# Performance work log

Hardware: AMD Instinct MI355X
Metric: run time of the kernel (lower is better)

The kernel has to match this reference:

```python
import jax, jax.numpy as jnp
import numpy as np

DMODEL = 1024
N_MAMBAS = 4
D_INNER = 2 * DMODEL          # expand = 2
D_STATE = 16                  # mamba_ssm default
D_CONV = 4                    # mamba_ssm default
DT_RANK = DMODEL // 16        # ceil(d_model/16) = 64


def setup_inputs() -> dict:
    key = jax.random.key(0)
    ks = jax.random.split(key, 8)
    B, L, n = 2, 4096, N_MAMBAS
    f32 = jnp.float32
    x = jax.random.normal(ks[0], (B, L, DMODEL), f32)
    in_w = jax.random.normal(ks[1], (n, 2 * D_INNER, DMODEL), f32) * 0.02
    conv_w = jax.random.normal(ks[2], (n, D_INNER, D_CONV), f32) * 0.1
    conv_b = jnp.zeros((n, D_INNER), f32)
    xproj_w = jax.random.normal(ks[3], (n, DT_RANK + 2 * D_STATE, D_INNER), f32) * 0.02
    dt_w = jax.random.normal(ks[4], (n, D_INNER, DT_RANK), f32) * 0.02
    # softplus-inverse of dt_init ~ 0.01 (mamba-style dt bias init)
    dt_b = jnp.log(jnp.expm1(jnp.full((n, D_INNER), 0.01, f32)))
    # S4D-real init: A_log = log(1..d_state)
    A_log = jnp.log(jnp.broadcast_to(jnp.arange(1, D_STATE + 1, dtype=f32), (n, D_INNER, D_STATE)))
    D_skip = jnp.ones((n, D_INNER), f32)
    out_w = jax.random.normal(ks[5], (n, DMODEL, D_INNER), f32) * 0.02
    return dict(x=x, in_w=in_w, conv_w=conv_w, conv_b=conv_b, xproj_w=xproj_w,
                dt_w=dt_w, dt_b=dt_b, A_log=A_log, D_skip=D_skip, out_w=out_w)


def _mamba(x, in_w, conv_w, conv_b, xproj_w, dt_w, dt_b, A_log, D_skip, out_w):
    # x: (B, Lc, D)
    Bb = x.shape[0]
    xz = jnp.einsum('bld,ed->ble', x, in_w)                 # (B, Lc, 2*D_INNER)
    xi, z = jnp.split(xz, 2, axis=-1)
    # causal depthwise conv over time
    xc = jnp.transpose(xi, (0, 2, 1))                       # (B, D_INNER, Lc)
    xc = jax.lax.conv_general_dilated(xc, conv_w[:, None, :], (1,),
                                      [(D_CONV - 1, 0)], feature_group_count=D_INNER)
    xi = jax.nn.silu(jnp.transpose(xc + conv_b[None, :, None], (0, 2, 1)))  # (B, Lc, D_INNER)
    proj = jnp.einsum('bld,ed->ble', xi, xproj_w)           # (B, Lc, DT_RANK + 2*D_STATE)
    dt = proj[..., :DT_RANK]
    Bm = proj[..., DT_RANK:DT_RANK + D_STATE]
    Cm = proj[..., DT_RANK + D_STATE:]
    dt = jax.nn.softplus(jnp.einsum('blr,dr->bld', dt, dt_w) + dt_b)  # (B, Lc, D_INNER)
    A = -jnp.exp(A_log)                                     # (D_INNER, D_STATE)

    def step(h, inp):
        dt_t, B_t, C_t, x_t = inp                           # (B,Di),(B,Ds),(B,Ds),(B,Di)
        dA = jnp.exp(dt_t[:, :, None] * A)                  # (B, Di, Ds)
        h = dA * h + dt_t[:, :, None] * B_t[:, None, :] * x_t[:, :, None]
        return h, jnp.einsum('bds,bs->bd', h, C_t)

    h0 = jnp.zeros((Bb, D_INNER, D_STATE), x.dtype)
    xs_t = (jnp.swapaxes(dt, 0, 1), jnp.swapaxes(Bm, 0, 1),
            jnp.swapaxes(Cm, 0, 1), jnp.swapaxes(xi, 0, 1))
    _, ys = jax.lax.scan(step, h0, xs_t)                    # (Lc, B, D_INNER)
    y = jnp.swapaxes(ys, 0, 1) + xi * D_skip                # (B, Lc, D_INNER)
    y = y * jax.nn.silu(z)
    return jnp.einsum('ble,de->bld', y, out_w)              # (B, Lc, D)


def reference(x, in_w, conv_w, conv_b, xproj_w, dt_w, dt_b, A_log, D_skip, out_w):
    B, L, D = x.shape
    n = N_MAMBAS
    # strided slices x[:, i::n] == reshape(B, L//n, n, D)[:, :, i]
    xs = jnp.transpose(x.reshape(B, L // n, n, D), (2, 0, 1, 3))   # (n, B, Lc, D)
    ys = jax.vmap(_mamba)(xs, in_w, conv_w, conv_b, xproj_w,
                          dt_w, dt_b, A_log, D_skip, out_w)        # (n, B, Lc, D)
    # torch.cat(dim=1) concatenates per-mamba outputs block-wise along seq
    return jnp.transpose(ys, (1, 0, 2, 3)).reshape(B, L, D)
```

## Files before the change

### kernel.cpp

```cpp
#include <hip/hip_runtime.h>
#include <math.h>

#define DM   1024
#define DI   2048
#define DSn  16
#define DTR  64
#define PW   96
#define LS   1024
#define NCH  16
#define CL   64
#define XKS  8

typedef unsigned short u16;
typedef unsigned int   u32;
typedef __attribute__((ext_vector_type(8))) short bf16x8;
typedef __attribute__((ext_vector_type(8))) unsigned short u16x8;
typedef __attribute__((ext_vector_type(4))) float f32x4;

__device__ __forceinline__ void split2(float f, u16& hi, u16& lo) {
  union { float f; unsigned int u; } v; v.f = f;
  hi = (u16)(v.u >> 16);
  union { unsigned int u; float f; } w; w.u = v.u & 0xffff0000u;
  union { float f; unsigned int u; } r; r.f = f - w.f;
  lo = (u16)(r.u >> 16);
}

template<int ROWS>
__device__ __forceinline__ bf16x8 frag(const u16* T, int l4, int row) {
  return *(const bf16x8*)&T[(l4 * ROWS + row) * 8];
}

template<int ROWS>
__device__ __forceinline__ void stage16f(const float* a, u16* Th, u16* Tl, int ra, int half) {
  #pragma unroll
  for (int q = 0; q < 2; ++q) {
    u16x8 vh, vl;
    #pragma unroll
    for (int c = 0; c < 8; ++c) {
      u16 h_, l_;
      split2(a[q * 8 + c], h_, l_);
      vh[c] = h_; vl[c] = l_;
    }
    const int slot = ((half * 2 + q) * ROWS + ra) * 8;
    *(u16x8*)&Th[slot] = vh;
    *(u16x8*)&Tl[slot] = vl;
  }
}

template<int ROWS>
__device__ __forceinline__ void stage8f(const float* a, u16* Th, u16* Tl, int rb, int kq) {
  u16x8 vh, vl;
  #pragma unroll
  for (int c = 0; c < 8; ++c) {
    u16 h_, l_;
    split2(a[c], h_, l_);
    vh[c] = h_; vl[c] = l_;
  }
  const int slot = (kq * ROWS + rb) * 8;
  *(u16x8*)&Th[slot] = vh;
  *(u16x8*)&Tl[slot] = vl;
}

__global__ __launch_bounds__(256) void k_split_x(
    const float* __restrict__ x, u16* __restrict__ xh, u16* __restrict__ xl, int ib0)
{
  const int idx = blockIdx.x * 256 + threadIdx.x;
  const int t = idx >> 8, kq = (idx & 255) * 4;
  const int gt = ib0 * 1024 + t;
  const int j = gt & (LS - 1), ib = gt >> 10;
  const int i = ib >> 1, bb = ib & 1;
  const float4 v = *(const float4*)&x[(size_t)(bb * 4096 + j * 4 + i) * DM + kq];
  ushort4 vh, vl;
  split2(v.x, vh.x, vl.x); split2(v.y, vh.y, vl.y);
  split2(v.z, vh.z, vl.z); split2(v.w, vh.w, vl.w);
  *(ushort4*)&xh[(size_t)t * DM + kq] = vh;
  *(ushort4*)&xl[(size_t)t * DM + kq] = vl;
}

__global__ __launch_bounds__(512) void k_inproj(
    const u16* __restrict__ xh, const u16* __restrict__ xl,
    const float* __restrict__ inwf,
    float* __restrict__ xz, int ib0, int swz)
{
  __shared__ __align__(16) u16 Ah[4*256*8], Al[4*256*8];
  __shared__ __align__(16) u16 Bh[4*128*8], Bl[4*128*8];
  const int tid = threadIdx.x;
  int mblk, nblk;
  if (swz) {
    const int o = blockIdx.x;
    const int xcd = o & 7, within = o >> 3;
    const int il_ = xcd >> 1, nh = xcd & 1;
    mblk = il_ * 8 + (within & 7);
    nblk = nh * 16 + (within >> 3);
  } else {
    mblk = blockIdx.x; nblk = blockIdx.y;
  }
  const int m0 = mblk << 8, n0 = nblk << 7;
  const int ib = ib0 + (m0 >> 10);
  const int il = (ib >> 1) - (ib0 >> 1);
  const int ra = tid >> 1, half = tid & 1;
  const u16* Aph = xh + (size_t)(m0 + ra) * DM + half * 16;
  const u16* Apl = xl + (size_t)(m0 + ra) * DM + half * 16;
  const int rb = tid >> 2, kq = tid & 3;
  const float* Bpf = inwf + ((size_t)il * 4096 + n0 + rb) * DM + kq * 8;
  const int w = tid >> 6, lane = tid & 63;
  const int wr = w >> 1, wc = w & 1;
  const int l15 = lane & 15, l4 = lane >> 4;

  f32x4 acc[4][4];
  #pragma unroll
  for (int a_ = 0; a_ < 4; ++a_)
    #pragma unroll
    for (int b_ = 0; b_ < 4; ++b_) acc[a_][b_] = (f32x4)(0.f);

  u16x8 pa[4];
  float br[8];
  pa[0] = *(const u16x8*)(Aph);     pa[1] = *(const u16x8*)(Aph + 8);
  pa[2] = *(const u16x8*)(Apl);     pa[3] = *(const u16x8*)(Apl + 8);
  *(f32x4*)&br[0] = *(const f32x4*)(Bpf);
  *(f32x4*)&br[4] = *(const f32x4*)(Bpf + 4);
  const int nk = DM / 32;
  for (int kt = 0; kt < nk; ++kt) {
    __syncthreads();
    *(u16x8*)&Ah[((half*2+0)*256 + ra)*8] = pa[0];
    *(u16x8*)&Ah[((half*2+1)*256 + ra)*8] = pa[1];
    *(u16x8*)&Al[((half*2+0)*256 + ra)*8] = pa[2];
    *(u16x8*)&Al[((half*2+1)*256 + ra)*8] = pa[3];
    stage8f<128>(br, Bh, Bl, rb, kq);
    __syncthreads();
    if (kt + 1 < nk) {
      const int k0 = (kt + 1) * 32;
      pa[0] = *(const u16x8*)(Aph + k0);     pa[1] = *(const u16x8*)(Aph + k0 + 8);
      pa[2] = *(const u16x8*)(Apl + k0);     pa[3] = *(const u16x8*)(Apl + k0 + 8);
      *(f32x4*)&br[0] = *(const f32x4*)(Bpf + k0);
      *(f32x4*)&br[4] = *(const f32x4*)(Bpf + k0 + 4);
    }
    bf16x8 ah[4], al[4];
    #pragma unroll
    for (int mf = 0; mf < 4; ++mf) {
      const int row = wr * 64 + mf * 16 + l15;
      ah[mf] = frag<256>(Ah, l4, row);
      al[mf] = frag<256>(Al, l4, row);
    }
    #pragma unroll
    for (int nf = 0; nf < 4; ++nf) {
      const int col = wc * 64 + nf * 16 + l15;
      bf16x8 bh = frag<128>(Bh, l4, col);
      bf16x8 bl = frag<128>(Bl, l4, col);
      #pragma unroll
      for (int mf = 0; mf < 4; ++mf) {
        acc[mf][nf] = __builtin_amdgcn_mfma_f32_16x16x32_bf16(ah[mf], bh, acc[mf][nf], 0, 0, 0);
        acc[mf][nf] = __builtin_amdgcn_mfma_f32_16x16x32_bf16(ah[mf], bl, acc[mf][nf], 0, 0, 0);
        acc[mf][nf] = __builtin_amdgcn_mfma_f32_16x16x32_bf16(al[mf], bh, acc[mf][nf], 0, 0, 0);
      }
    }
  }
  #pragma unroll
  for (int mf = 0; mf < 4; ++mf) {
    const int row = m0 + wr * 64 + mf * 16 + l4 * 4;
    #pragma unroll
    for (int nf = 0; nf < 4; ++nf) {
      const int col = n0 + wc * 64 + nf * 16 + l15;
      #pragma unroll
      for (int r = 0; r < 4; ++r)
        xz[(size_t)(row + r) * (2 * DI) + col] = acc[mf][nf][r];
    }
  }
}

__global__ __launch_bounds__(256) void k_conv(
    const float* __restrict__ xz, const float* __restrict__ convw,
    const float* __restrict__ convb, float* __restrict__ xib,
    int ib0, int ntok)
{
  const int idx = blockIdx.x * 256 + threadIdx.x;
  if (idx >= ntok * (DI / 4)) return;
  const int t = idx / (DI / 4);
  const int c = (idx - t * (DI / 4)) * 4;
  const int j = t & (LS - 1);
  const int i = (ib0 + (t >> 10)) >> 1;
  float4 acc = *(const float4*)&convb[(size_t)i * DI + c];
  float4 wt[4];
  #pragma unroll
  for (int q = 0; q < 4; ++q)
    wt[q] = *(const float4*)&convw[((size_t)i * DI + c + q) * 4];
  #pragma unroll
  for (int k = 0; k < 4; ++k) {
    const int j2 = j + k - 3;
    if (j2 >= 0) {
      const float4 v = *(const float4*)&xz[(size_t)(t + k - 3) * (2 * DI) + c];
      acc.x = fmaf(v.x, ((const float*)&wt[0])[k], acc.x);
      acc.y = fmaf(v.y, ((const float*)&wt[1])[k], acc.y);
      acc.z = fmaf(v.z, ((const float*)&wt[2])[k], acc.z);
      acc.w = fmaf(v.w, ((const float*)&wt[3])[k], acc.w);
    }
  }
  float4 o;
  o.x = acc.x / (1.f + __expf(-acc.x));
  o.y = acc.y / (1.f + __expf(-acc.y));
  o.z = acc.z / (1.f + __expf(-acc.z));
  o.w = acc.w / (1.f + __expf(-acc.w));
  *(float4*)&xib[(size_t)t * DI + c] = o;
}

__global__ __launch_bounds__(256) void k_xproj_part(
    const float* __restrict__ xif, const float* __restrict__ xwf,
    float* __restrict__ Pp, int ib0, int ntok)
{
  __shared__ __align__(16) u16 Ah[4*64*8], Al[4*64*8];
  __shared__ __align__(16) u16 Bh[4*96*8], Bl[4*96*8];
  const int tid = threadIdx.x;
  const int m0 = blockIdx.x << 6;
  const int ks = blockIdx.y;
  const int kbase = ks * (DI / XKS);
  const int ib = ib0 + (m0 >> 10);
  const int il = (ib >> 1) - (ib0 >> 1);
  const int ra = tid >> 1, half = tid & 1;
  const bool hasA = (tid < 128);
  const bool hasB = (tid < 192);
  const float* Apf = xif + (size_t)(m0 + ra) * DI + kbase + half * 16;
  const float* Bpf = xwf + ((size_t)il * PW + ra) * DI + kbase + half * 16;
  const int w = tid >> 6, lane = tid & 63;
  const int l15 = lane & 15, l4 = lane >> 4;

  f32x4 acc[6];
  #pragma unroll
  for (int b_ = 0; b_ < 6; ++b_) acc[b_] = (f32x4)(0.f);

  float ar[16], br[16];
  if (hasA) {
    #pragma unroll
    for (int q = 0; q < 4; ++q) *(f32x4*)&ar[q*4] = *(const f32x4*)(Apf + q*4);
  }
  if (hasB) {
    #pragma unroll
    for (int q = 0; q < 4; ++q) *(f32x4*)&br[q*4] = *(const f32x4*)(Bpf + q*4);
  }
  const int nk = (DI / XKS) / 32;
  for (int kt = 0; kt < nk; ++kt) {
    __syncthreads();
    if (hasA) stage16f<64>(ar, Ah, Al, ra, half);
    if (hasB) stage16f<96>(br, Bh, Bl, ra, half);
    __syncthreads();
    if (kt + 1 < nk) {
      const int k0 = (kt + 1) * 32;
      if (hasA) {
        #pragma unroll
        for (int q = 0; q < 4; ++q) *(f32x4*)&ar[q*4] = *(const f32x4*)(Apf + k0 + q*4);
      }
      if (hasB) {
        #pragma unroll
        for (int q = 0; q < 4; ++q) *(f32x4*)&br[q*4] = *(const f32x4*)(Bpf + k0 + q*4);
      }
    }
    const int arow = w * 16 + l15;
    bf16x8 ah = frag<64>(Ah, l4, arow);
    bf16x8 al = frag<64>(Al, l4, arow);
    #pragma unroll
    for (int nf = 0; nf < 6; ++nf) {
      const int col = nf * 16 + l15;
      bf16x8 bh = frag<96>(Bh, l4, col);
      bf16x8 bl = frag<96>(Bl, l4, col);
      acc[nf] = __builtin_amdgcn_mfma_f32_16x16x32_bf16(ah, bh, acc[nf], 0, 0, 0);
      acc[nf] = __builtin_amdgcn_mfma_f32_16x16x32_bf16(ah, bl, acc[nf], 0, 0, 0);
      acc[nf] = __builtin_amdgcn_mfma_f32_16x16x32_bf16(al, bh, acc[nf], 0, 0, 0);
    }
  }
  float* outp = Pp + (size_t)ks * ntok * PW;
  const int row = m0 + w * 16 + l4 * 4;
  #pragma unroll
  for (int nf = 0; nf < 6; ++nf) {
    const int col = nf * 16 + l15;
    #pragma unroll
    for (int r = 0; r < 4; ++r)
      outp[(size_t)(row + r) * PW + col] = acc[nf][r];
  }
}

__global__ __launch_bounds__(256) void k_xproj_red(
    const float* __restrict__ Pp, float* __restrict__ projb, int ntok)
{
  const int idx = blockIdx.x * 256 + threadIdx.x;
  if (idx >= ntok * PW) return;
  const size_t plane = (size_t)ntok * PW;
  float s = 0.f;
  #pragma unroll
  for (int ks = 0; ks < XKS; ++ks) s += Pp[(size_t)ks * plane + idx];
  projb[idx] = s;
}

__global__ __launch_bounds__(256) void k_dtproj(
    const float* __restrict__ proj, const float* __restrict__ dtw,
    const float* __restrict__ dtbias, float* __restrict__ dtout,
    int dstride, int ib0)
{
  __shared__ float As[16][132];
  __shared__ float Bs[16][132];
  const int tid = threadIdx.x;
  const int n0 = blockIdx.x << 7;
  const int m0 = blockIdx.y << 7;
  const int ib = ib0 + (m0 >> 10);
  const int i  = ib >> 1;
  const int ar = tid >> 2, kq = tid & 3;
  const float* A0 = proj + (size_t)(m0 + ar) * PW + kq * 4;
  const float* A1 = A0 + (size_t)64 * PW;
  const float* Wb = dtw + (size_t)i * DI * DTR;
  const float* B0 = Wb + (size_t)(n0 + ar) * DTR + kq * 4;
  const float* B1 = B0 + (size_t)64 * DTR;
  const int tx = tid & 15, ty = tid >> 4;
  float acc[8][8] = {};
  for (int kt = 0; kt < DTR / 16; ++kt) {
    const int k0 = kt * 16;
    float4 a0 = *(const float4*)(A0 + k0);
    float4 a1 = *(const float4*)(A1 + k0);
    float4 b0 = *(const float4*)(B0 + k0);
    float4 b1 = *(const float4*)(B1 + k0);
    __syncthreads();
    As[kq*4+0][ar] = a0.x; As[kq*4+1][ar] = a0.y; As[kq*4+2][ar] = a0.z; As[kq*4+3][ar] = a0.w;
    As[kq*4+0][ar+64] = a1.x; As[kq*4+1][ar+64] = a1.y; As[kq*4+2][ar+64] = a1.z; As[kq*4+3][ar+64] = a1.w;
    Bs[kq*4+0][ar] = b0.x; Bs[kq*4+1][ar] = b0.y; Bs[kq*4+2][ar] = b0.z; Bs[kq*4+3][ar] = b0.w;
    Bs[kq*4+0][ar+64] = b1.x; Bs[kq*4+1][ar+64] = b1.y; Bs[kq*4+2][ar+64] = b1.z; Bs[kq*4+3][ar+64] = b1.w;
    __syncthreads();
    #pragma unroll
    for (int k = 0; k < 16; ++k) {
      const float4 av0 = *(const float4*)&As[k][ty*8];
      const float4 av1 = *(const float4*)&As[k][ty*8+4];
      const float4 bv0 = *(const float4*)&Bs[k][tx*8];
      const float4 bv1 = *(const float4*)&Bs[k][tx*8+4];
      const float aa[8] = {av0.x,av0.y,av0.z,av0.w,av1.x,av1.y,av1.z,av1.w};
      const float bv[8] = {bv0.x,bv0.y,bv0.z,bv0.w,bv1.x,bv1.y,bv1.z,bv1.w};
      #pragma unroll
      for (int r = 0; r < 8; ++r)
        #pragma unroll
        for (int c = 0; c < 8; ++c)
          acc[r][c] = fmaf(aa[r], bv[c], acc[r][c]);
    }
  }
  float bias[8];
  #pragma unroll
  for (int c = 0; c < 8; ++c) bias[c] = dtbias[(size_t)i * DI + n0 + tx*8 + c];
  #pragma unroll
  for (int r = 0; r < 8; ++r) {
    const int t = m0 + ty*8 + r;
    #pragma unroll
    for (int c = 0; c < 8; ++c) {
      float u = acc[r][c] + bias[c];
      float sp = (u > 20.f) ? u : log1pf(__expf(u));
      dtout[(size_t)t * dstride + n0 + tx*8 + c] = sp;
    }
  }
}

__global__ __launch_bounds__(256) void k_scan_part(
    const float* __restrict__ projb, const float* dtp, int dstride,
    const float* __restrict__ xib, const float* __restrict__ A_log,
    float* __restrict__ Pbuf, float* __restrict__ Hbuf, int ib0)
{
  const int d = blockIdx.x * 256 + threadIdx.x;
  const int ch = blockIdx.y, lib = blockIdx.z;
  const int i = (ib0 + lib) >> 1;
  const size_t gd = (size_t)i * DI + d;
  __shared__ float bs[CL][DSn];
  const size_t trow = (size_t)lib * LS + (size_t)ch * CL;
  for (int p = threadIdx.x; p < CL * DSn; p += 256) {
    const int jj = p >> 4, ss = p & 15;
    bs[jj][ss] = projb[(trow + jj) * PW + DTR + ss];
  }
  float A[DSn], P[DSn], h[DSn];
  #pragma unroll
  for (int s = 0; s < DSn; ++s) {
    A[s] = -__expf(A_log[gd * DSn + s]);
    P[s] = 1.f; h[s] = 0.f;
  }
  __syncthreads();
  float dt_c = dtp[trow * dstride + d];
  float xi_c = xib[trow * DI + d];
  for (int j = 0; j < CL; ++j) {
    float dt_n = 0.f, xi_n = 0.f;
    if (j + 1 < CL) {
      dt_n = dtp[(trow + j + 1) * dstride + d];
      xi_n = xib[(trow + j + 1) * DI + d];
    }
    const float dx = dt_c * xi_c;
    #pragma unroll
    for (int s = 0; s < DSn; ++s) {
      const float dA = __expf(dt_c * A[s]);
      P[s] *= dA;
      h[s] = fmaf(dA, h[s], dx * bs[j][s]);
    }
    dt_c = dt_n; xi_c = xi_n;
  }
  const size_t base = ((size_t)(lib * NCH + ch) * DSn) * DI + d;
  #pragma unroll
  for (int s = 0; s < DSn; ++s) {
    Pbuf[base + (size_t)s * DI] = P[s];
    Hbuf[base + (size_t)s * DI] = h[s];
  }
}

__global__ __launch_bounds__(256) void k_scan_mid(
    float* __restrict__ Pbuf, const float* __restrict__ Hbuf, int nib)
{
  const int idx = blockIdx.x * 256 + threadIdx.x;
  if (idx >= nib * DSn * DI) return;
  const int d = idx & (DI - 1);
  const int s = (idx >> 11) & 15;
  const int lib = idx >> 15;
  const size_t stride = (size_t)DSn * DI;
  const size_t base = ((size_t)lib * NCH * DSn + s) * DI + d;
  float carry = 0.f;
  for (int c = 0; c < NCH; ++c) {
    const size_t o = base + (size_t)c * stride;
    const float p = Pbuf[o];
    const float hl = Hbuf[o];
    Pbuf[o] = carry;
    carry = fmaf(p, carry, hl);
  }
}

__global__ __launch_bounds__(256) void k_scan_full(
    const float* __restrict__ projb, const float* dtp, int dstride,
    float* xibio, const float* xzz,
    const float* __restrict__ A_log, const float* __restrict__ D_skip,
    const float* __restrict__ Pbuf, int ib0)
{
  const int d = blockIdx.x * 256 + threadIdx.x;
  const int ch = blockIdx.y, lib = blockIdx.z;
  const int i = (ib0 + lib) >> 1;
  const size_t gd = (size_t)i * DI + d;
  __shared__ float bs[CL][2 * DSn];
  const size_t trow = (size_t)lib * LS + (size_t)ch * CL;
  for (int p = threadIdx.x; p < CL * 2 * DSn; p += 256) {
    const int jj = p >> 5, ss = p & 31;
    bs[jj][ss] = projb[(trow + jj) * PW + DTR + ss];
  }
  float A[DSn], h[DSn];
  const size_t hbase = ((size_t)(lib * NCH + ch) * DSn) * DI + d;
  #pragma unroll
  for (int s = 0; s < DSn; ++s) {
    A[s] = -__expf(A_log[gd * DSn + s]);
    h[s] = Pbuf[hbase + (size_t)s * DI];
  }
  const float Dsk = D_skip[gd];
  __syncthreads();
  float dt_c = dtp[trow * dstride + d];
  float xi_c = xibio[trow * DI + d];
  float z_c  = xzz[trow * (2 * DI) + DI + d];
  for (int j = 0; j < CL; ++j) {
    float dt_n = 0.f, xi_n = 0.f, z_n = 0.f;
    if (j + 1 < CL) {
      dt_n = dtp[(trow + j + 1) * dstride + d];
      xi_n = xibio[(trow + j + 1) * DI + d];
      z_n  = xzz[(trow + j + 1) * (2 * DI) + DI + d];
    }
    const float dx = dt_c * xi_c;
    float y = 0.f;
    #pragma unroll
    for (int s = 0; s < DSn; ++s) {
      const float dA = __expf(dt_c * A[s]);
      h[s] = fmaf(dA, h[s], dx * bs[j][s]);
      y = fmaf(h[s], bs[j][DSn + s], y);
    }
    const float sz = z_c / (1.f + __expf(-z_c));
    const float val = (y + xi_c * Dsk) * sz;
    u16 vh, vl;
    split2(val, vh, vl);
    ((u32*)xibio)[(trow + j) * DI + d] = ((u32)vh << 16) | (u32)vl;
    dt_c = dt_n; xi_c = xi_n; z_c = z_n;
  }
}

__global__ __launch_bounds__(256) void k_outproj(
    const u32* __restrict__ ybp, const float* __restrict__ owf,
    float* __restrict__ out, int ib0)
{
  __shared__ __align__(16) u16 Ah[4*128*8], Al[4*128*8];
  __shared__ __align__(16) u16 Bh[4*128*8], Bl[4*128*8];
  const int tid = threadIdx.x;
  const int m0 = blockIdx.x << 7;
  const int n0 = blockIdx.y << 7;
  const int ib = ib0 + (m0 >> 10);
  const int i = ib >> 1, bb = ib & 1;
  const int il = i - (ib0 >> 1);
  const int ra = tid >> 1, half = tid & 1;
  const u32* Ap = ybp + (size_t)(m0 + ra) * DI + half * 16;
  const int rb = tid >> 1;
  const float* Bpf = owf + ((size_t)il * DM + n0 + rb) * DI + half * 16;
  const int w = tid >> 6, lane = tid & 63;
  const int wr = w >> 1, wc = w & 1;
  const int l15 = lane & 15, l4 = lane >> 4;

  f32x4 acc[4][4];
  #pragma unroll
  for (int a_ = 0; a_ < 4; ++a_)
    #pragma unroll
    for (int b_ = 0; b_ < 4; ++b_) acc[a_][b_] = (f32x4)(0.f);

  uint4 qa[4];
  float br[16];
  qa[0] = *(const uint4*)(Ap);     qa[1] = *(const uint4*)(Ap + 4);
  qa[2] = *(const uint4*)(Ap + 8); qa[3] = *(const uint4*)(Ap + 12);
  #pragma unroll
  for (int q = 0; q < 4; ++q) *(f32x4*)&br[q*4] = *(const f32x4*)(Bpf + q*4);
  const int nk = DI / 32;
  for (int kt = 0; kt < nk; ++kt) {
    __syncthreads();
    #pragma unroll
    for (int g = 0; g < 2; ++g) {
      const u32 e[8] = { qa[2*g].x, qa[2*g].y, qa[2*g].z, qa[2*g].w,
                         qa[2*g+1].x, qa[2*g+1].y, qa[2*g+1].z, qa[2*g+1].w };
      u16x8 vh, vl;
      #pragma unroll
      for (int c = 0; c < 8; ++c) { vh[c] = (u16)(e[c] >> 16); vl[c] = (u16)(e[c] & 0xffffu); }
      const int slot = ((half*2+g)*128 + ra)*8;
      *(u16x8*)&Ah[slot] = vh;
      *(u16x8*)&Al[slot] = vl;
    }
    stage16f<128>(br, Bh, Bl, rb, half);
    __syncthreads();
    if (kt + 1 < nk) {
      const int k0 = (kt + 1) * 32;
      qa[0] = *(const uint4*)(Ap + k0);     qa[1] = *(const uint4*)(Ap + k0 + 4);
      qa[2] = *(const uint4*)(Ap + k0 + 8); qa[3] = *(const uint4*)(Ap + k0 + 12);
      #pragma unroll
      for (int q = 0; q < 4; ++q) *(f32x4*)&br[q*4] = *(const f32x4*)(Bpf + k0 + q*4);
    }
    bf16x8 ah[4], al[4];
    #pragma unroll
    for (int mf = 0; mf < 4; ++mf) {
      const int row = wr * 64 + mf * 16 + l15;
      ah[mf] = frag<128>(Ah, l4, row);
      al[mf] = frag<128>(Al, l4, row);
    }
    #pragma unroll
    for (int nf = 0; nf < 4; ++nf) {
      const int col = wc * 64 + nf * 16 + l15;
      bf16x8 bh = frag<128>(Bh, l4, col);
      bf16x8 bl = frag<128>(Bl, l4, col);
      #pragma unroll
      for (int mf = 0; mf < 4; ++mf) {
        acc[mf][nf] = __builtin_amdgcn_mfma_f32_16x16x32_bf16(ah[mf], bh, acc[mf][nf], 0, 0, 0);
        acc[mf][nf] = __builtin_amdgcn_mfma_f32_16x16x32_bf16(ah[mf], bl, acc[mf][nf], 0, 0, 0);
        acc[mf][nf] = __builtin_amdgcn_mfma_f32_16x16x32_bf16(al[mf], bh, acc[mf][nf], 0, 0, 0);
      }
    }
  }
  #pragma unroll
  for (int mf = 0; mf < 4; ++mf) {
    const int t0 = m0 + wr * 64 + mf * 16 + l4 * 4;
    #pragma unroll
    for (int nf = 0; nf < 4; ++nf) {
      const int col = n0 + wc * 64 + nf * 16 + l15;
      #pragma unroll
      for (int r = 0; r < 4; ++r) {
        const int j = (t0 + r) & (LS - 1);
        out[(size_t)(bb * 4096 + i * 1024 + j) * DM + col] = acc[mf][nf][r];
      }
    }
  }
}

extern "C" void kernel_launch(void* const* d_in, const int* in_sizes, int n_in,
                              void* d_out, int out_size, void* d_ws, size_t ws_size,
                              hipStream_t stream) {
  (void)in_sizes; (void)n_in; (void)out_size;
  const float* x       = (const float*)d_in[0];
  const float* in_w    = (const float*)d_in[1];
  const float* conv_w  = (const float*)d_in[2];
  const float* conv_b  = (const float*)d_in[3];
  const float* xproj_w = (const float*)d_in[4];
  const float* dt_w    = (const float*)d_in[5];
  const float* dt_b    = (const float*)d_in[6];
  const float* A_log   = (const float*)d_in[7];
  const float* D_skip  = (const float*)d_in[8];
  const float* out_w   = (const float*)d_in[9];
  float* out = (float*)d_out;
  const dim3 blk(256);

  const size_t needSP = ((size_t)8192 * 4096 + (size_t)8192 * 2048 + (size_t)8192 * 96) * 4;
  if (ws_size >= needSP) {
    const size_t nt = 8192;
    float* xz    = (float*)d_ws;
    float* xib   = xz + nt * (2 * DI);
    float* projb = xib + nt * DI;
    u16* xph  = (u16*)d_out;  u16* xpl  = xph + nt * DM;
    float* Pp = (float*)d_out;
    float* Pbuf = (float*)d_out;
    float* Hbuf = Pbuf + (size_t)8 * NCH * DSn * DI;
    float* dtz = xz;
    u32* ybp  = (u32*)xib;

    k_split_x<<<dim3((int)nt), blk, 0, stream>>>(x, xph, xpl, 0);
    k_inproj<<<dim3(1024), dim3(512), 0, stream>>>(xph, xpl, in_w, xz, 0, 1);
    k_conv<<<dim3((int)(nt*(DI/4)/256)), blk, 0, stream>>>(xz, conv_w, conv_b, xib, 0, (int)nt);
    k_xproj_part<<<dim3((int)(nt/64), XKS), blk, 0, stream>>>(xib, xproj_w, Pp, 0, (int)nt);
    k_xproj_red<<<dim3((int)(nt*PW/256)), blk, 0, stream>>>(Pp, projb, (int)nt);
    k_dtproj<<<dim3(DI/128, (int)(nt/128)), blk, 0, stream>>>(projb, dt_w, dt_b, dtz, 2*DI, 0);
    k_scan_part<<<dim3(DI/256, NCH, 8), blk, 0, stream>>>(projb, dtz, 2*DI, xib, A_log, Pbuf, Hbuf, 0);
    k_scan_mid<<<dim3(8 * DSn * DI / 256), blk, 0, stream>>>(Pbuf, Hbuf, 8);
    k_scan_full<<<dim3(DI/256, NCH, 8), blk, 0, stream>>>(projb, dtz, 2*DI, xib, xz, A_log, D_skip, Pbuf, 0);
    k_outproj<<<dim3((int)(nt/128), 8), blk, 0, stream>>>(ybp, out_w, out, 0);
    return;
  }

  auto needFB = [](int nib) -> size_t { return (size_t)nib * 29753344ull; };
  const int step = (ws_size >= needFB(4)) ? 4 : 2;

  for (int ib0 = 0; ib0 < 8; ib0 += step) {
    const int nib = step;
    const size_t nt = (size_t)nib * LS;
    const int i0 = ib0 >> 1;
    float* xz    = (float*)d_ws;
    float* xib   = xz + nt * (2 * DI);
    float* projb = xib + nt * DI;
    float* SH    = projb + nt * PW;
    u16* xph  = (u16*)SH;  u16* xpl = xph + nt * DM;
    float* Pp = SH;
    float* Pbuf = SH;
    float* Hbuf = Pbuf + (size_t)nib * NCH * DSn * DI / 2;
    float* dtz = xz;
    u32* ybp  = (u32*)xib;

    k_split_x<<<dim3((int)nt), blk, 0, stream>>>(x, xph, xpl, ib0);
    k_inproj<<<dim3((int)(nt/256), 32), dim3(512), 0, stream>>>(xph, xpl, in_w + (size_t)i0*4096*DM, xz, ib0, 0);
    k_conv<<<dim3((int)(nt*(DI/4)/256)), blk, 0, stream>>>(xz, conv_w, conv_b, xib, ib0, (int)nt);
    k_xproj_part<<<dim3((int)(nt/64), XKS), blk, 0, stream>>>(xib, xproj_w + (size_t)i0*PW*DI, Pp, ib0, (int)nt);
    k_xproj_red<<<dim3((int)(nt*PW/256)), blk, 0, stream>>>(Pp, projb, (int)nt);
    k_dtproj<<<dim3(DI/128, (int)(nt/128)), blk, 0, stream>>>(projb, dt_w, dt_b, dtz, 2*DI, ib0);
    k_scan_part<<<dim3(DI/256, NCH, nib), blk, 0, stream>>>(projb, dtz, 2*DI, xib, A_log, Pbuf, Hbuf, ib0);
    k_scan_mid<<<dim3(nib * DSn * DI / 256), blk, 0, stream>>>(Pbuf, Hbuf, nib);
    k_scan_full<<<dim3(DI/256, NCH, nib), blk, 0, stream>>>(projb, dtz, 2*DI, xib, xz, A_log, D_skip, Pbuf, ib0);
    k_outproj<<<dim3((int)(nt/128), 8), blk, 0, stream>>>(ybp, out_w + (size_t)i0*DM*DI, out, ib0);
  }
}
```

Before: 644.8 us.

## Enlarge in-proj GEMM tile to 256x256 with double-buffered padded LDS

The in-projection GEMM tile grows from 256x128 to 256x256, with 8 waves laid out 2x4 and each wave holding 8x4 accumulator fragments. LDS becomes a double-buffered, padded layout, so each k-step needs one barrier instead of two, and the next global load is issued two steps ahead. The grid is halved and the XCD swizzle remapped to match. The goal is less global traffic per MFMA and less sync overhead, at the cost of much higher register pressure (128 accumulator floats per thread plus 16 prefetched B floats) and more LDS per block. That could lower occupancy or cause spills, and the launch_bounds(512,2) hint may not be met.

```diff
diff --git a/kernel.cpp b/kernel.cpp
--- a/kernel.cpp
+++ b/kernel.cpp
@@ -77,87 +77,109 @@
   *(ushort4*)&xl[(size_t)t * DM + kq] = vl;
 }
 
-__global__ __launch_bounds__(512) void k_inproj(
+#define KGP 2064
+__global__ __launch_bounds__(512, 2) void k_inproj(
     const u16* __restrict__ xh, const u16* __restrict__ xl,
     const float* __restrict__ inwf,
     float* __restrict__ xz, int ib0, int swz)
 {
-  __shared__ __align__(16) u16 Ah[4*256*8], Al[4*256*8];
-  __shared__ __align__(16) u16 Bh[4*128*8], Bl[4*128*8];
+  __shared__ __align__(16) u16 L[2][4][4][KGP];
   const int tid = threadIdx.x;
   int mblk, nblk;
   if (swz) {
     const int o = blockIdx.x;
     const int xcd = o & 7, within = o >> 3;
-    const int il_ = xcd >> 1, nh = xcd & 1;
-    mblk = il_ * 8 + (within & 7);
-    nblk = nh * 16 + (within >> 3);
+    mblk = xcd * 4 + (within & 3);
+    nblk = within >> 2;
   } else {
     mblk = blockIdx.x; nblk = blockIdx.y;
   }
-  const int m0 = mblk << 8, n0 = nblk << 7;
+  const int m0 = mblk << 8, n0 = nblk << 8;
   const int ib = ib0 + (m0 >> 10);
   const int il = (ib >> 1) - (ib0 >> 1);
   const int ra = tid >> 1, half = tid & 1;
   const u16* Aph = xh + (size_t)(m0 + ra) * DM + half * 16;
   const u16* Apl = xl + (size_t)(m0 + ra) * DM + half * 16;
-  const int rb = tid >> 2, kq = tid & 3;
-  const float* Bpf = inwf + ((size_t)il * 4096 + n0 + rb) * DM + kq * 8;
+  const float* Bpf = inwf + ((size_t)il * 4096 + n0 + ra) * DM + half * 16;
   const int w = tid >> 6, lane = tid & 63;
-  const int wr = w >> 1, wc = w & 1;
+  const int wr = w >> 2, wc = w & 3;
   const int l15 = lane & 15, l4 = lane >> 4;
 
-  f32x4 acc[4][4];
-  #pragma unroll
-  for (int a_ = 0; a_ < 4; ++a_)
+  f32x4 acc[8][4];
+  #pragma unroll
+  for (int a_ = 0; a_ < 8; ++a_)
     #pragma unroll
     for (int b_ = 0; b_ < 4; ++b_) acc[a_][b_] = (f32x4)(0.f);
 
-  u16x8 pa[4];
-  float br[8];
-  pa[0] = *(const u16x8*)(Aph);     pa[1] = *(const u16x8*)(Aph + 8);
-  pa[2] = *(const u16x8*)(Apl);     pa[3] = *(const u16x8*)(Apl + 8);
-  *(f32x4*)&br[0] = *(const f32x4*)(Bpf);
-  *(f32x4*)&br[4] = *(const f32x4*)(Bpf + 4);
-  const int nk = DM / 32;
-  for (int kt = 0; kt < nk; ++kt) {
-    __syncthreads();
-    *(u16x8*)&Ah[((half*2+0)*256 + ra)*8] = pa[0];
-    *(u16x8*)&Ah[((half*2+1)*256 + ra)*8] = pa[1];
-    *(u16x8*)&Al[((half*2+0)*256 + ra)*8] = pa[2];
-    *(u16x8*)&Al[((half*2+1)*256 + ra)*8] = pa[3];
-    stage8f<128>(br, Bh, Bl, rb, kq);
-    __syncthreads();
-    if (kt + 1 < nk) {
-      const int k0 = (kt + 1) * 32;
-      pa[0] = *(const u16x8*)(Aph + k0);     pa[1] = *(const u16x8*)(Aph + k0 + 8);
-      pa[2] = *(const u16x8*)(Apl + k0);     pa[3] = *(const u16x8*)(Apl + k0 + 8);
-      *(f32x4*)&br[0] = *(const f32x4*)(Bpf + k0);
-      *(f32x4*)&br[4] = *(const f32x4*)(Bpf + k0 + 4);
-    }
-    bf16x8 ah[4], al[4];
-    #pragma unroll
-    for (int mf = 0; mf < 4; ++mf) {
-      const int row = wr * 64 + mf * 16 + l15;
-      ah[mf] = frag<256>(Ah, l4, row);
-      al[mf] = frag<256>(Al, l4, row);
-    }
+  u16x8 ah2[2], al2[2];
+  float br[16];
+
+  auto LOADG = [&](int kt) {
+    const int k0 = kt * 32;
+    ah2[0] = *(const u16x8*)(Aph + k0);
+    ah2[1] = *(const u16x8*)(Aph + k0 + 8);
+    al2[0] = *(const u16x8*)(Apl + k0);
+    al2[1] = *(const u16x8*)(Apl + k0 + 8);
+    *(f32x4*)&br[0]  = *(const f32x4*)(Bpf + k0);
+    *(f32x4*)&br[4]  = *(const f32x4*)(Bpf + k0 + 4);
+    *(f32x4*)&br[8]  = *(const f32x4*)(Bpf + k0 + 8);
+    *(f32x4*)&br[12] = *(const f32x4*)(Bpf + k0 + 12);
+  };
+  auto STORE = [&](int b) {
+    #pragma unroll
+    for (int q = 0; q < 2; ++q) {
+      const int kg = half * 2 + q;
+      *(u16x8*)&L[b][0][kg][ra * 8] = ah2[q];
+      *(u16x8*)&L[b][1][kg][ra * 8] = al2[q];
+      u16x8 vh, vl;
+      #pragma unroll
+      for (int c = 0; c < 8; ++c) {
+        u16 h_, l_;
+        split2(br[q * 8 + c], h_, l_);
+        vh[c] = h_; vl[c] = l_;
+      }
+      *(u16x8*)&L[b][2][kg][ra * 8] = vh;
+      *(u16x8*)&L[b][3][kg][ra * 8] = vl;
+    }
+  };
+  auto COMPUTE = [&](int b) {
+    bf16x8 bh[4], bl[4];
     #pragma unroll
     for (int nf = 0; nf < 4; ++nf) {
       const int col = wc * 64 + nf * 16 + l15;
-      bf16x8 bh = frag<128>(Bh, l4, col);
-      bf16x8 bl = frag<128>(Bl, l4, col);
-      #pragma unroll
-      for (int mf = 0; mf < 4; ++mf) {
-        acc[mf][nf] = __builtin_amdgcn_mfma_f32_16x16x32_bf16(ah[mf], bh, acc[mf][nf], 0, 0, 0);
-        acc[mf][nf] = __builtin_amdgcn_mfma_f32_16x16x32_bf16(ah[mf], bl, acc[mf][nf], 0, 0, 0);
-        acc[mf][nf] = __builtin_amdgcn_mfma_f32_16x16x32_bf16(al[mf], bh, acc[mf][nf], 0, 0, 0);
+      bh[nf] = *(const bf16x8*)&L[b][2][l4][col * 8];
+      bl[nf] = *(const bf16x8*)&L[b][3][l4][col * 8];
+    }
+    #pragma unroll
+    for (int mf = 0; mf < 8; ++mf) {
+      const int row = wr * 128 + mf * 16 + l15;
+      bf16x8 ah = *(const bf16x8*)&L[b][0][l4][row * 8];
+      bf16x8 al = *(const bf16x8*)&L[b][1][l4][row * 8];
+      #pragma unroll
+      for (int nf = 0; nf < 4; ++nf) {
+        acc[mf][nf] = __builtin_amdgcn_mfma_f32_16x16x32_bf16(ah, bh[nf], acc[mf][nf], 0, 0, 0);
+        acc[mf][nf] = __builtin_amdgcn_mfma_f32_16x16x32_bf16(ah, bl[nf], acc[mf][nf], 0, 0, 0);
+        acc[mf][nf] = __builtin_amdgcn_mfma_f32_16x16x32_bf16(al, bh[nf], acc[mf][nf], 0, 0, 0);
       }
     }
-  }
-  #pragma unroll
-  for (int mf = 0; mf < 4; ++mf) {
-    const int row = m0 + wr * 64 + mf * 16 + l4 * 4;
+  };
+
+  const int nk = DM / 32;
+  LOADG(0);
+  STORE(0);
+  if (nk > 1) LOADG(1);
+  __syncthreads();
+  for (int kt = 0; kt < nk; ++kt) {
+    const int c = kt & 1;
+    if (kt + 1 < nk) STORE(c ^ 1);
+    if (kt + 2 < nk) LOADG(kt + 2);
+    COMPUTE(c);
+    __syncthreads();
+  }
+
+  #pragma unroll
+  for (int mf = 0; mf < 8; ++mf) {
+    const int row = m0 + wr * 128 + mf * 16 + l4 * 4;
     #pragma unroll
     for (int nf = 0; nf < 4; ++nf) {
       const int col = n0 + wc * 64 + nf * 16 + l15;
@@ -591,7 +613,7 @@
     u32* ybp  = (u32*)xib;
 
     k_split_x<<<dim3((int)nt), blk, 0, stream>>>(x, xph, xpl, 0);
-    k_inproj<<<dim3(1024), dim3(512), 0, stream>>>(xph, xpl, in_w, xz, 0, 1);
+    k_inproj<<<dim3(512), dim3(512), 0, stream>>>(xph, xpl, in_w, xz, 0, 1);
     k_conv<<<dim3((int)(nt*(DI/4)/256)), blk, 0, stream>>>(xz, conv_w, conv_b, xib, 0, (int)nt);
     k_xproj_part<<<dim3((int)(nt/64), XKS), blk, 0, stream>>>(xib, xproj_w, Pp, 0, (int)nt);
     k_xproj_red<<<dim3((int)(nt*PW/256)), blk, 0, stream>>>(Pp, projb, (int)nt);
@@ -622,7 +644,7 @@
     u32* ybp  = (u32*)xib;
 
     k_split_x<<<dim3((int)nt), blk, 0, stream>>>(x, xph, xpl, ib0);
-    k_inproj<<<dim3((int)(nt/256), 32), dim3(512), 0, stream>>>(xph, xpl, in_w + (size_t)i0*4096*DM, xz, ib0, 0);
+    k_inproj<<<dim3((int)(nt/256), 16), dim3(512), 0, stream>>>(xph, xpl, in_w + (size_t)i0*4096*DM, xz, ib0, 0);
     k_conv<<<dim3((int)(nt*(DI/4)/256)), blk, 0, stream>>>(xz, conv_w, conv_b, xib, ib0, (int)nt);
     k_xproj_part<<<dim3((int)(nt/64), XKS), blk, 0, stream>>>(xib, xproj_w + (size_t)i0*PW*DI, Pp, ib0, (int)nt);
     k_xproj_red<<<dim3((int)(nt*PW/256)), blk, 0, stream>>>(Pp, projb, (int)nt);
```

After: 627.9 us. 2.6% less time.
